# Kernel tuning notes

Hardware: AMD Instinct MI355X
Metric: run time of the kernel (lower is better)

Reference implementation:

```python
import jax, jax.numpy as jnp
import numpy as np

D_MODEL = 1280
N_HEADS = 16
DEPTH = D_MODEL // N_HEADS  # 80
NEG_BIG = -10000.0


def setup_inputs() -> dict:
    key = jax.random.key(0)
    ks = jax.random.split(key, 12)
    B, S = 2, 2048
    std = 1.0 / np.sqrt(D_MODEL)
    inp = {
        "v": jax.random.normal(ks[0], (B, S, D_MODEL), jnp.float32),
        "k": jax.random.normal(ks[1], (B, S, D_MODEL), jnp.float32),
        "q": jax.random.normal(ks[2], (B, S, D_MODEL), jnp.float32),
        # causal mask: 1.0 on strictly-upper triangle (future positions)
        "mask": jnp.triu(jnp.ones((S, S), jnp.float32), k=1),
        "Wq_w": jax.random.normal(ks[3], (D_MODEL, D_MODEL), jnp.float32) * std,
        "Wq_b": jnp.zeros((D_MODEL,), jnp.float32),
        "Wk_w": jax.random.normal(ks[4], (D_MODEL, D_MODEL), jnp.float32) * std,
        "Wk_b": jnp.zeros((D_MODEL,), jnp.float32),
        "Wv_w": jax.random.normal(ks[5], (D_MODEL, D_MODEL), jnp.float32) * std,
        "Wv_b": jnp.zeros((D_MODEL,), jnp.float32),
        "dense_w": jax.random.normal(ks[6], (D_MODEL, D_MODEL), jnp.float32) * std,
        "dense_b": jnp.zeros((D_MODEL,), jnp.float32),
    }
    return inp


def _split_heads(x, B):
    # [B, S, D] -> [B, H, S, depth]
    return x.reshape(B, -1, N_HEADS, DEPTH).transpose(0, 2, 1, 3)


def reference(v, k, q, mask, Wq_w, Wq_b, Wk_w, Wk_b, Wv_w, Wv_b, dense_w, dense_b):
    B = q.shape[0]
    # torch Linear: y = x @ W.T + b
    qh = _split_heads(q @ Wq_w.T + Wq_b, B)
    kh = _split_heads(k @ Wk_w.T + Wk_b, B)
    vh = _split_heads(v @ Wv_w.T + Wv_b, B)

    scale = 1.0 / np.sqrt(DEPTH)
    logits = jnp.einsum("bhqd,bhkd->bhqk", qh, kh) * scale  # [B,H,S,S]
    nd, ns = logits.shape[-2], logits.shape[-1]
    logits = logits + mask[ns - nd:ns, :ns] * NEG_BIG
    attn = jax.nn.softmax(logits, axis=-1)
    out = jnp.einsum("bhqk,bhkd->bhqd", attn, vh)  # [B,H,S,depth]
    out = out.transpose(0, 2, 1, 3).reshape(B, -1, D_MODEL)
    out = out @ dense_w.T + dense_b
    return out, attn
```

## Files before the change

kernel.cpp:

```cpp
#include <hip/hip_runtime.h>
#include <hip/hip_bf16.h>

typedef short frag8 __attribute__((ext_vector_type(8)));
typedef float facc4 __attribute__((ext_vector_type(4)));
typedef float f32x4 __attribute__((ext_vector_type(4)));
typedef unsigned short ushort_t;
typedef unsigned int uint_t;

#define DEV static __device__ __forceinline__

DEV ushort_t f2bf(float f) {
  uint_t u = __float_as_uint(f);
  u += 0x7fffu + ((u >> 16) & 1u);
  return (ushort_t)(u >> 16);
}
DEV uint_t cvt_pk(float lo, float hi) {
  uint_t r;
  asm("v_cvt_pk_bf16_f32 %0, %1, %2" : "=v"(r) : "v"(lo), "v"(hi));
  return r;
}
DEV frag8 pack8(float4 a, float4 b) {
  union { frag8 f; uint4 u; } u_;
  u_.u.x = cvt_pk(a.x, a.y); u_.u.y = cvt_pk(a.z, a.w);
  u_.u.z = cvt_pk(b.x, b.y); u_.u.w = cvt_pk(b.z, b.w);
  return u_.f;
}
DEV void bar_lds() { asm volatile("s_waitcnt lgkmcnt(0)\n\ts_barrier" ::: "memory"); }

constexpr int B_ = 2, S_ = 2048, H_ = 16, DM = 1280, DH = 80, DP = 96;
constexpr size_t IN_E = (size_t)B_ * S_ * DM;
constexpr size_t WT_E = (size_t)DM * DM;
constexpr size_t OFF_WQ = 0;
constexpr size_t OFF_WK = OFF_WQ + WT_E;
constexpr size_t OFF_WV = OFF_WK + WT_E;
constexpr size_t OFF_WD = OFF_WV + WT_E;
constexpr size_t QH_E  = (size_t)B_ * H_ * S_ * DP;
constexpr size_t OFF_QH = OFF_WD + WT_E;
constexpr size_t OFF_KH = OFF_QH + QH_E;
constexpr size_t VT_E  = (size_t)B_ * H_ * DH * S_;
constexpr size_t OFF_VT = OFF_KH + QH_E;
constexpr size_t OFF_OH = OFF_VT + VT_E;

constexpr float QSCALE = 0.16129822f;

__global__ void convert_kernel(const float* __restrict__ wq, const float* __restrict__ wk,
                               const float* __restrict__ wv, const float* __restrict__ wd,
                               ushort_t* __restrict__ ws) {
  size_t i = (size_t)blockIdx.x * blockDim.x + threadIdx.x;
  size_t stride = (size_t)gridDim.x * blockDim.x;
  constexpr size_t TOTAL = 4 * WT_E / 8;
  constexpr size_t NROW = (size_t)B_ * H_ * S_;
  constexpr size_t PADC = 2 * NROW * 2;
  for (size_t c = i; c < TOTAL + PADC; c += stride) {
    if (c < TOTAL) {
      size_t e = c * 8;
      const float* s2; size_t lo;
      if      (e < WT_E)     { s2 = wq; lo = e; }
      else if (e < 2 * WT_E) { s2 = wk; lo = e - WT_E; }
      else if (e < 3 * WT_E) { s2 = wv; lo = e - 2 * WT_E; }
      else                   { s2 = wd; lo = e - 3 * WT_E; }
      float4 a = *(const float4*)(s2 + lo);
      float4 b = *(const float4*)(s2 + lo + 4);
      uint4 o;
      o.x = (uint_t)f2bf(a.x) | ((uint_t)f2bf(a.y) << 16);
      o.y = (uint_t)f2bf(a.z) | ((uint_t)f2bf(a.w) << 16);
      o.z = (uint_t)f2bf(b.x) | ((uint_t)f2bf(b.y) << 16);
      o.w = (uint_t)f2bf(b.z) | ((uint_t)f2bf(b.w) << 16);
      *(uint4*)(ws + e) = o;
    } else {
      size_t rr = c - TOTAL;
      size_t row = rr >> 1;
      size_t base = (row < NROW ? OFF_QH : OFF_KH) + (row & (NROW - 1)) * DP + DH + (rr & 1) * 8;
      uint4 z = {0u, 0u, 0u, 0u};
      *(uint4*)(ws + base) = z;
    }
  }
}

__global__ __launch_bounds__(256) void qkv_kernel(const float* __restrict__ Aq,
                                                  const float* __restrict__ Ak,
                                                  const float* __restrict__ Av,
                                                  const ushort_t* __restrict__ wts,
                                                  const float* __restrict__ bq,
                                                  const float* __restrict__ bk,
                                                  const float* __restrict__ bv,
                                                  ushort_t* __restrict__ qh_o,
                                                  ushort_t* __restrict__ kh_o,
                                                  ushort_t* __restrict__ vt_o) {
  __shared__ __align__(16) ushort_t sA[2][128][40];
  __shared__ __align__(16) ushort_t sB[2][128][40];
  int which = blockIdx.x / 320;
  int local = blockIdx.x - which * 320;
  int swz = (local & 7) * 40 + (local >> 3);
  int tm = swz / 10, tn = swz % 10;
  int m0 = tm * 128, n0 = tn * 128;
  const float* A = which == 0 ? Aq : which == 1 ? Ak : Av;
  const ushort_t* W = wts + (size_t)which * WT_E;
  const float* bias = which == 0 ? bq : which == 1 ? bk : bv;
  int tid = threadIdx.x, l = tid & 63, wv = tid >> 6;
  int lm = l & 15, lg = l >> 4;
  int wr = wv >> 1, wc = wv & 1;
  int srow = tid >> 2, schk = tid & 3;
  facc4 acc[4][4] = {};
  frag8 ra[2], rb[2];

  auto load_tile = [&](int kt) {
    const float* Ab = A + (size_t)(m0 + srow) * DM + kt * 32 + schk * 8;
    ra[0] = pack8(*(const float4*)Ab, *(const float4*)(Ab + 4));
    const float* Ab2 = Ab + (size_t)64 * DM;
    ra[1] = pack8(*(const float4*)Ab2, *(const float4*)(Ab2 + 4));
    const ushort_t* Bb = W + (size_t)(n0 + srow) * DM + kt * 32 + schk * 8;
    rb[0] = *(const frag8*)Bb;
    rb[1] = *(const frag8*)(Bb + (size_t)64 * DM);
  };
  auto store_tile = [&](int bb) {
    *(frag8*)&sA[bb][srow][schk * 8] = ra[0];
    *(frag8*)&sA[bb][srow + 64][schk * 8] = ra[1];
    *(frag8*)&sB[bb][srow][schk * 8] = rb[0];
    *(frag8*)&sB[bb][srow + 64][schk * 8] = rb[1];
  };

  load_tile(0);
  store_tile(0);
  __syncthreads();
  for (int kt = 0; kt < 40; ++kt) {
    int cur = kt & 1;
    if (kt < 39) load_tile(kt + 1);
    frag8 af[4], bf[4];
#pragma unroll
    for (int i = 0; i < 4; ++i) af[i] = *(const frag8*)&sA[cur][wr * 64 + i * 16 + lm][lg * 8];
#pragma unroll
    for (int i = 0; i < 4; ++i) bf[i] = *(const frag8*)&sB[cur][wc * 64 + i * 16 + lm][lg * 8];
#pragma unroll
    for (int mi = 0; mi < 4; ++mi)
#pragma unroll
      for (int ni = 0; ni < 4; ++ni)
        acc[mi][ni] = __builtin_amdgcn_mfma_f32_16x16x32_bf16(af[mi], bf[ni], acc[mi][ni], 0, 0, 0);
    if (kt < 39) store_tile(cur ^ 1);
    __syncthreads();
  }

  float scale = (which == 0) ? QSCALE : 1.0f;
  ushort_t* dst = which == 0 ? qh_o : which == 1 ? kh_o : vt_o;
#pragma unroll
  for (int ni = 0; ni < 4; ++ni) {
    int n = n0 + wc * 64 + ni * 16 + lm;
    float bv2 = bias[n];
    int h = n / 80, d = n % 80;
#pragma unroll
    for (int mi = 0; mi < 4; ++mi) {
      int mbase = m0 + wr * 64 + mi * 16 + lg * 4;
      int b = mbase >> 11, sp = mbase & 2047;
      if (which < 2) {
#pragma unroll
        for (int r = 0; r < 4; ++r) {
          float vl = (acc[mi][ni][r] + bv2) * scale;
          dst[((size_t)(b * H_ + h) * S_ + sp + r) * DP + d] = f2bf(vl);
        }
      } else {
        uint2 u2;
        u2.x = cvt_pk(acc[mi][ni][0] + bv2, acc[mi][ni][1] + bv2);
        u2.y = cvt_pk(acc[mi][ni][2] + bv2, acc[mi][ni][3] + bv2);
        *(uint2*)&dst[((size_t)(b * H_ + h) * DH + d) * S_ + sp] = u2;
      }
    }
  }
}

__global__ __launch_bounds__(256) void dense_kernel(const ushort_t* __restrict__ A,
                                                    const ushort_t* __restrict__ W,
                                                    const float* __restrict__ bias,
                                                    float* __restrict__ dst_f) {
  __shared__ __align__(16) ushort_t sA[2][128][40];
  __shared__ __align__(16) ushort_t sB[2][128][40];
  int bid = blockIdx.x;
  int swz = (bid & 7) * 40 + (bid >> 3);
  int tm = swz / 10, tn = swz % 10;
  int m0 = tm * 128, n0 = tn * 128;
  int tid = threadIdx.x, l = tid & 63, wv = tid >> 6;
  int lm = l & 15, lg = l >> 4;
  int wr = wv >> 1, wc = wv & 1;
  int srow = tid >> 2, schk = tid & 3;
  facc4 acc[4][4] = {};
  frag8 ra[2], rb[2];

  auto load_tile = [&](int kt) {
    const ushort_t* Ab = A + (size_t)(m0 + srow) * DM + kt * 32 + schk * 8;
    ra[0] = *(const frag8*)Ab;
    ra[1] = *(const frag8*)(Ab + (size_t)64 * DM);
    const ushort_t* Bb = W + (size_t)(n0 + srow) * DM + kt * 32 + schk * 8;
    rb[0] = *(const frag8*)Bb;
    rb[1] = *(const frag8*)(Bb + (size_t)64 * DM);
  };
  auto store_tile = [&](int bb) {
    *(frag8*)&sA[bb][srow][schk * 8] = ra[0];
    *(frag8*)&sA[bb][srow + 64][schk * 8] = ra[1];
    *(frag8*)&sB[bb][srow][schk * 8] = rb[0];
    *(frag8*)&sB[bb][srow + 64][schk * 8] = rb[1];
  };

  load_tile(0);
  store_tile(0);
  __syncthreads();
  for (int kt = 0; kt < 40; ++kt) {
    int cur = kt & 1;
    if (kt < 39) load_tile(kt + 1);
    frag8 af[4], bf[4];
#pragma unroll
    for (int i = 0; i < 4; ++i) af[i] = *(const frag8*)&sA[cur][wr * 64 + i * 16 + lm][lg * 8];
#pragma unroll
    for (int i = 0; i < 4; ++i) bf[i] = *(const frag8*)&sB[cur][wc * 64 + i * 16 + lm][lg * 8];
#pragma unroll
    for (int mi = 0; mi < 4; ++mi)
#pragma unroll
      for (int ni = 0; ni < 4; ++ni)
        acc[mi][ni] = __builtin_amdgcn_mfma_f32_16x16x32_bf16(af[mi], bf[ni], acc[mi][ni], 0, 0, 0);
    if (kt < 39) store_tile(cur ^ 1);
    __syncthreads();
  }

#pragma unroll
  for (int ni = 0; ni < 4; ++ni) {
    int n = n0 + wc * 64 + ni * 16 + lm;
    float bv2 = bias[n];
#pragma unroll
    for (int mi = 0; mi < 4; ++mi) {
      int mbase = m0 + wr * 64 + mi * 16 + lg * 4;
#pragma unroll
      for (int r = 0; r < 4; ++r)
        __builtin_nontemporal_store(acc[mi][ni][r] + bv2, dst_f + (size_t)(mbase + r) * DM + n);
    }
  }
}

__global__ __launch_bounds__(512, 4) void attn_kernel(const ushort_t* __restrict__ qh,
                                                      const ushort_t* __restrict__ kh,
                                                      const ushort_t* __restrict__ vt,
                                                      ushort_t* __restrict__ outh,
                                                      float* __restrict__ out_attn) {
  __shared__ __align__(16) ushort_t sK[2][64][104];
  __shared__ __align__(16) ushort_t sV[2][80][68];
  __shared__ __align__(16) char sP[8 * 2048];
  int bid = blockIdx.x;
  int half = bid >> 8, rr0 = bid & 255;
  int swz = (rr0 & 7) * 32 + (rr0 >> 3);
  int bh = swz >> 3, pr = swz & 7;
  int b = bh >> 4, h = bh & 15;
  int s = half ? (15 - pr) : pr;
  int tid = threadIdx.x, w = tid >> 6, l = tid & 63, lm = l & 15, lg = l >> 4;
  const ushort_t* qhb = qh + (size_t)bh * S_ * DP;
  const ushort_t* khb = kh + (size_t)bh * S_ * DP;
  const ushort_t* vtb = vt + (size_t)bh * DH * S_;
  float* attnb = out_attn + (size_t)bh * S_ * S_;
  char* Pw = sP + w * 2048;

  int sr[3], sc[3];
#pragma unroll
  for (int i = 0; i < 3; ++i) {
    int c = tid * 3 + i;
    sr[i] = c / 24; sc[i] = (c % 24) * 4;
  }
  uint2 stk[3];
  auto ldtK = [&](int t) {
#pragma unroll
    for (int i = 0; i < 3; ++i)
      stk[i] = *(const uint2*)(khb + (size_t)(t * 64 + sr[i]) * DP + sc[i]);
  };
  auto sttK = [&](int bb) {
#pragma unroll
    for (int i = 0; i < 3; ++i)
      *(uint2*)&sK[bb][sr[i]][sc[i]] = stk[i];
  };
  int vrow = tid >> 3, vcol = (tid & 7) * 8;
  uint4 stv0, stv1;
  auto ldtV = [&](int t) {
    stv0 = *(const uint4*)(vtb + (size_t)vrow * S_ + t * 64 + vcol);
    if (tid < 128) stv1 = *(const uint4*)(vtb + (size_t)(64 + vrow) * S_ + t * 64 + vcol);
  };
  auto sttV = [&](int bb) {
    *(uint4*)&sV[bb][vrow][vcol] = stv0;
    if (tid < 128) *(uint4*)&sV[bb][64 + vrow][vcol] = stv1;
  };

  int q0 = s * 128;
  int wq0 = q0 + w * 16;
  int qg = wq0 + lm;

  if (s < 15) {
    int c0 = (s + 1) * 128;
    int r2 = tid >> 2;
    int l4 = (tid & 3) << 2;
    float* rowp = attnb + (size_t)(q0 + r2) * S_ + c0 + l4;
    f32x4 z = {0.f, 0.f, 0.f, 0.f};
    for (int cc = 0; cc < 2048 - c0; cc += 16)
      __builtin_nontemporal_store(z, (f32x4*)(rowp + cc));
  }

  frag8 qf[3];
#pragma unroll
  for (int kd = 0; kd < 3; ++kd)
    qf[kd] = *(const frag8*)(qhb + (size_t)qg * DP + kd * 32 + lg * 8);
  int NT = 2 * (s + 1);

  float rs4[4] = {0.f, 0.f, 0.f, 0.f};
  {
    int NT1 = 2 * s + 1 + (w >> 2);
    for (int t = 0; t < NT1; ++t) {
      const ushort_t* kp = khb + (size_t)t * 64 * DP;
      facc4 acc[4] = {};
#pragma unroll
      for (int mi = 0; mi < 4; ++mi)
#pragma unroll
        for (int kd = 0; kd < 3; ++kd) {
          frag8 af = *(const frag8*)(kp + (size_t)(mi * 16 + lm) * DP + kd * 32 + lg * 8);
          acc[mi] = __builtin_amdgcn_mfma_f32_16x16x32_bf16(af, qf[kd], acc[mi], 0, 0, 0);
        }
      if (64 * t + 63 <= wq0) {
#pragma unroll
        for (int mi = 0; mi < 4; ++mi)
#pragma unroll
          for (int r = 0; r < 4; ++r) rs4[r] += exp2f(acc[mi][r]);
      } else {
#pragma unroll
        for (int mi = 0; mi < 4; ++mi)
#pragma unroll
          for (int r = 0; r < 4; ++r) {
            int kg = t * 64 + mi * 16 + lg * 4 + r;
            if (kg <= qg) rs4[r] += exp2f(acc[mi][r]);
          }
      }
    }
  }
  float rs = (rs4[0] + rs4[1]) + (rs4[2] + rs4[3]);
  rs += __shfl_xor(rs, 16);
  rs += __shfl_xor(rs, 32);
  float li = -__log2f(rs);

  facc4 acc2[5] = {};
  ldtK(0); ldtV(0); sttK(0); sttV(0);
  if (NT > 1) { ldtK(1); ldtV(1); }
  bar_lds();
  for (int t = 0; t < NT; ++t) {
    int cur = t & 1;
    if (t + 1 < NT) { sttK(cur ^ 1); sttV(cur ^ 1); }
    if (t + 2 < NT) { ldtK(t + 2); ldtV(t + 2); }
    if (64 * t >= wq0 + 16) {
      f32x4 z = {0.f, 0.f, 0.f, 0.f};
#pragma unroll
      for (int mi = 0; mi < 4; ++mi)
        *(f32x4*)(attnb + (size_t)qg * S_ + t * 64 + mi * 16 + lg * 4) = z;
    } else {
      facc4 acc[4] = {};
#pragma unroll
      for (int mi = 0; mi < 4; ++mi)
#pragma unroll
        for (int kd = 0; kd < 3; ++kd) {
          frag8 af = *(const frag8*)((const char*)sK + cur * (64 * 104 * 2) +
                                     (mi * 16 + lm) * 208 + kd * 64 + lg * 16);
          acc[mi] = __builtin_amdgcn_mfma_f32_16x16x32_bf16(af, qf[kd], acc[mi], 0, 0, 0);
        }
      bool full = (64 * t + 63 <= wq0);
#pragma unroll
      for (int mi = 0; mi < 4; ++mi) {
        float p[4];
        if (full) {
#pragma unroll
          for (int r = 0; r < 4; ++r) p[r] = exp2f(acc[mi][r] + li);
        } else {
#pragma unroll
          for (int r = 0; r < 4; ++r) {
            int kg = t * 64 + mi * 16 + lg * 4 + r;
            p[r] = (kg <= qg) ? exp2f(acc[mi][r] + li) : 0.f;
          }
        }
        f32x4 f4 = {p[0], p[1], p[2], p[3]};
        *(f32x4*)(attnb + (size_t)qg * S_ + t * 64 + mi * 16 + lg * 4) = f4;
        uint2 pk;
        pk.x = cvt_pk(p[0], p[1]);
        pk.y = cvt_pk(p[2], p[3]);
        int kb = mi * 32 + lg * 8;
        *(uint2*)(Pw + lm * 128 + (kb ^ ((lm & 7) << 4))) = pk;
      }
#pragma unroll
      for (int ks = 0; ks < 2; ++ks) {
        int kbyte = ks * 64 + lg * 16;
        frag8 pa = *(const frag8*)(Pw + lm * 128 + (kbyte ^ ((lm & 7) << 4)));
#pragma unroll
        for (int nf = 0; nf < 5; ++nf) {
          frag8 vb = *(const frag8*)&sV[cur][nf * 16 + lm][ks * 32 + lg * 8];
          acc2[nf] = __builtin_amdgcn_mfma_f32_16x16x32_bf16(pa, vb, acc2[nf], 0, 0, 0);
        }
      }
    }
    bar_lds();
  }
#pragma unroll
  for (int nf = 0; nf < 5; ++nf)
#pragma unroll
    for (int r = 0; r < 4; ++r) {
      int qrow = q0 + w * 16 + lg * 4 + r;
      int col = h * DH + nf * 16 + lm;
      outh[((size_t)b * S_ + qrow) * DM + col] = f2bf(acc2[nf][r]);
    }
}

extern "C" void kernel_launch(void* const* d_in, const int* in_sizes, int n_in,
                              void* d_out, int out_size, void* d_ws, size_t ws_size,
                              hipStream_t stream) {
  const float* v  = (const float*)d_in[0];
  const float* k  = (const float*)d_in[1];
  const float* q  = (const float*)d_in[2];
  const float* wq = (const float*)d_in[4];
  const float* bq = (const float*)d_in[5];
  const float* wk = (const float*)d_in[6];
  const float* bk = (const float*)d_in[7];
  const float* wv = (const float*)d_in[8];
  const float* bv = (const float*)d_in[9];
  const float* wd = (const float*)d_in[10];
  const float* bd = (const float*)d_in[11];
  ushort_t* ws = (ushort_t*)d_ws;
  float* out  = (float*)d_out;
  float* attn = out + IN_E;

  convert_kernel<<<2048, 256, 0, stream>>>(wq, wk, wv, wd, ws);
  qkv_kernel<<<960, 256, 0, stream>>>(q, k, v, ws + OFF_WQ, bq, bk, bv,
                                      ws + OFF_QH, ws + OFF_KH, ws + OFF_VT);
  attn_kernel<<<512, 512, 0, stream>>>(ws + OFF_QH, ws + OFF_KH, ws + OFF_VT, ws + OFF_OH, attn);
  dense_kernel<<<320, 256, 0, stream>>>(ws + OFF_OH, ws + OFF_WD, bd, out);
}
```

Before: 374.3 us.

## Stage K tiles through shared LDS for row-sum pass and defer zero-fill stores

The first (row-sum) pass over K now loads 128-row K tiles cooperatively into a double-buffered region of a unified LDS buffer, instead of having each wave read K fragments directly from global memory. This shares K reads across the eight waves and overlaps the next tile's global loads with MFMA work. The zero-fill of the masked upper triangle of the attention output is moved to the end of the kernel so those stores no longer delay the start of compute. It adds barriers to the first pass and aliases the LDS regions of the two passes, which must not overlap while in use.

```diff
diff --git a/kernel.cpp b/kernel.cpp
--- a/kernel.cpp
+++ b/kernel.cpp
@@ -238,9 +238,10 @@
                                                       const ushort_t* __restrict__ vt,
                                                       ushort_t* __restrict__ outh,
                                                       float* __restrict__ out_attn) {
-  __shared__ __align__(16) ushort_t sK[2][64][104];
-  __shared__ __align__(16) ushort_t sV[2][80][68];
-  __shared__ __align__(16) char sP[8 * 2048];
+  __shared__ __align__(16) char sLDS[64768];
+  ushort_t (*K2)[64][104] = (ushort_t(*)[64][104])sLDS;
+  ushort_t (*V2)[80][68]  = (ushort_t(*)[80][68])(sLDS + 26624);
+  char* sPb = sLDS + 48384;
   int bid = blockIdx.x;
   int half = bid >> 8, rr0 = bid & 255;
   int swz = (rr0 & 7) * 32 + (rr0 >> 3);
@@ -252,7 +253,7 @@
   const ushort_t* khb = kh + (size_t)bh * S_ * DP;
   const ushort_t* vtb = vt + (size_t)bh * DH * S_;
   float* attnb = out_attn + (size_t)bh * S_ * S_;
-  char* Pw = sP + w * 2048;
+  char* Pw = sPb + w * 2048;
 
   int sr[3], sc[3];
 #pragma unroll
@@ -269,7 +270,22 @@
   auto sttK = [&](int bb) {
 #pragma unroll
     for (int i = 0; i < 3; ++i)
-      *(uint2*)&sK[bb][sr[i]][sc[i]] = stk[i];
+      *(uint2*)&K2[bb][sr[i]][sc[i]] = stk[i];
+  };
+  uint2 stk6[6];
+  auto ldtK1 = [&](int t1) {
+#pragma unroll
+    for (int i = 0; i < 6; ++i) {
+      int c = tid * 6 + i;
+      stk6[i] = *(const uint2*)(khb + (size_t)(t1 * 128 + c / 24) * DP + (c % 24) * 4);
+    }
+  };
+  auto sttK1 = [&](int bb) {
+#pragma unroll
+    for (int i = 0; i < 6; ++i) {
+      int c = tid * 6 + i;
+      *(uint2*)(sLDS + bb * 26624 + (c / 24) * 208 + (c % 24) * 8) = stk6[i];
+    }
   };
   int vrow = tid >> 3, vcol = (tid & 7) * 8;
   uint4 stv0, stv1;
@@ -278,24 +294,14 @@
     if (tid < 128) stv1 = *(const uint4*)(vtb + (size_t)(64 + vrow) * S_ + t * 64 + vcol);
   };
   auto sttV = [&](int bb) {
-    *(uint4*)&sV[bb][vrow][vcol] = stv0;
-    if (tid < 128) *(uint4*)&sV[bb][64 + vrow][vcol] = stv1;
+    *(uint4*)&V2[bb][vrow][vcol] = stv0;
+    if (tid < 128) *(uint4*)&V2[bb][64 + vrow][vcol] = stv1;
   };
 
   int q0 = s * 128;
   int wq0 = q0 + w * 16;
   int qg = wq0 + lm;
 
-  if (s < 15) {
-    int c0 = (s + 1) * 128;
-    int r2 = tid >> 2;
-    int l4 = (tid & 3) << 2;
-    float* rowp = attnb + (size_t)(q0 + r2) * S_ + c0 + l4;
-    f32x4 z = {0.f, 0.f, 0.f, 0.f};
-    for (int cc = 0; cc < 2048 - c0; cc += 16)
-      __builtin_nontemporal_store(z, (f32x4*)(rowp + cc));
-  }
-
   frag8 qf[3];
 #pragma unroll
   for (int kd = 0; kd < 3; ++kd)
@@ -304,31 +310,43 @@
 
   float rs4[4] = {0.f, 0.f, 0.f, 0.f};
   {
-    int NT1 = 2 * s + 1 + (w >> 2);
-    for (int t = 0; t < NT1; ++t) {
-      const ushort_t* kp = khb + (size_t)t * 64 * DP;
-      facc4 acc[4] = {};
-#pragma unroll
-      for (int mi = 0; mi < 4; ++mi)
-#pragma unroll
-        for (int kd = 0; kd < 3; ++kd) {
-          frag8 af = *(const frag8*)(kp + (size_t)(mi * 16 + lm) * DP + kd * 32 + lg * 8);
-          acc[mi] = __builtin_amdgcn_mfma_f32_16x16x32_bf16(af, qf[kd], acc[mi], 0, 0, 0);
+    int T1 = s + 1;
+    ldtK1(0); sttK1(0);
+    if (T1 > 1) ldtK1(1);
+    bar_lds();
+    for (int t1 = 0; t1 < T1; ++t1) {
+      int cur = t1 & 1;
+      if (t1 + 1 < T1) sttK1(cur ^ 1);
+      if (t1 + 2 < T1) ldtK1(t1 + 2);
+#pragma unroll
+      for (int hf = 0; hf < 2; ++hf) {
+        int t = 2 * t1 + hf;
+        if (64 * t >= wq0 + 16) break;
+        facc4 acc[4] = {};
+#pragma unroll
+        for (int mi = 0; mi < 4; ++mi)
+#pragma unroll
+          for (int kd = 0; kd < 3; ++kd) {
+            frag8 af = *(const frag8*)(sLDS + cur * 26624 +
+                                       (hf * 64 + mi * 16 + lm) * 208 + kd * 64 + lg * 16);
+            acc[mi] = __builtin_amdgcn_mfma_f32_16x16x32_bf16(af, qf[kd], acc[mi], 0, 0, 0);
+          }
+        if (64 * t + 63 <= wq0) {
+#pragma unroll
+          for (int mi = 0; mi < 4; ++mi)
+#pragma unroll
+            for (int r = 0; r < 4; ++r) rs4[r] += exp2f(acc[mi][r]);
+        } else {
+#pragma unroll
+          for (int mi = 0; mi < 4; ++mi)
+#pragma unroll
+            for (int r = 0; r < 4; ++r) {
+              int kg = t * 64 + mi * 16 + lg * 4 + r;
+              if (kg <= qg) rs4[r] += exp2f(acc[mi][r]);
+            }
         }
-      if (64 * t + 63 <= wq0) {
-#pragma unroll
-        for (int mi = 0; mi < 4; ++mi)
-#pragma unroll
-          for (int r = 0; r < 4; ++r) rs4[r] += exp2f(acc[mi][r]);
-      } else {
-#pragma unroll
-        for (int mi = 0; mi < 4; ++mi)
-#pragma unroll
-          for (int r = 0; r < 4; ++r) {
-            int kg = t * 64 + mi * 16 + lg * 4 + r;
-            if (kg <= qg) rs4[r] += exp2f(acc[mi][r]);
-          }
       }
+      bar_lds();
     }
   }
   float rs = (rs4[0] + rs4[1]) + (rs4[2] + rs4[3]);
@@ -355,7 +373,7 @@
       for (int mi = 0; mi < 4; ++mi)
 #pragma unroll
         for (int kd = 0; kd < 3; ++kd) {
-          frag8 af = *(const frag8*)((const char*)sK + cur * (64 * 104 * 2) +
+          frag8 af = *(const frag8*)(sLDS + cur * 13312 +
                                      (mi * 16 + lm) * 208 + kd * 64 + lg * 16);
           acc[mi] = __builtin_amdgcn_mfma_f32_16x16x32_bf16(af, qf[kd], acc[mi], 0, 0, 0);
         }
@@ -387,7 +405,7 @@
         frag8 pa = *(const frag8*)(Pw + lm * 128 + (kbyte ^ ((lm & 7) << 4)));
 #pragma unroll
         for (int nf = 0; nf < 5; ++nf) {
-          frag8 vb = *(const frag8*)&sV[cur][nf * 16 + lm][ks * 32 + lg * 8];
+          frag8 vb = *(const frag8*)&V2[cur][nf * 16 + lm][ks * 32 + lg * 8];
           acc2[nf] = __builtin_amdgcn_mfma_f32_16x16x32_bf16(pa, vb, acc2[nf], 0, 0, 0);
         }
       }
@@ -402,6 +420,16 @@
       int col = h * DH + nf * 16 + lm;
       outh[((size_t)b * S_ + qrow) * DM + col] = f2bf(acc2[nf][r]);
     }
+
+  if (s < 15) {
+    int c0 = (s + 1) * 128;
+    int r2 = tid >> 2;
+    int l4 = (tid & 3) << 2;
+    float* rowp = attnb + (size_t)(q0 + r2) * S_ + c0 + l4;
+    f32x4 z = {0.f, 0.f, 0.f, 0.f};
+    for (int cc = 0; cc < 2048 - c0; cc += 16)
+      __builtin_nontemporal_store(z, (f32x4*)(rowp + cc));
+  }
 }
 
 extern "C" void kernel_launch(void* const* d_in, const int* in_sizes, int n_in,
```

Measured after the change: 330.3 us. -11.8%, faster.
